# Optimization experiments

Measured on AMD Instinct MI355X. Metric: run time of the kernel, lower is better.

## Reference

```python
import jax, jax.numpy as jnp
import numpy as np

H = 768
NH = 12
HD = H // NH  # 64


def setup_inputs() -> dict:
    key = jax.random.key(0)
    ks = jax.random.split(key, 8)
    B, S = 4, 2048
    sc = 1.0 / np.sqrt(H)
    return {
        "hidden_states": jax.random.normal(ks[0], (B, S, H), dtype=jnp.float32),
        "attention_mask": jnp.zeros((B, 1, 1, S), dtype=jnp.float32),
        "Wq": jax.random.normal(ks[1], (H, H), dtype=jnp.float32) * sc,
        "bq": jnp.zeros((H,), dtype=jnp.float32),
        "Wk": jax.random.normal(ks[2], (H, H), dtype=jnp.float32) * sc,
        "bk": jnp.zeros((H,), dtype=jnp.float32),
        "Wv": jax.random.normal(ks[3], (H, H), dtype=jnp.float32) * sc,
        "bv": jnp.zeros((H,), dtype=jnp.float32),
    }


def _split_heads(x):
    # [B,S,H] -> [B,NH,S,HD]
    B, S, _ = x.shape
    return x.reshape(B, S, NH, HD).transpose(0, 2, 1, 3)


def reference(hidden_states, attention_mask, Wq, bq, Wk, bk, Wv, bv):
    q = _split_heads(hidden_states @ Wq + bq)
    k = _split_heads(hidden_states @ Wk + bk)
    v = _split_heads(hidden_states @ Wv + bv)
    # scores: [B,NH,S,S]
    scores = jnp.einsum("bhqd,bhkd->bhqk", q, k) / np.sqrt(HD)
    scores = scores + attention_mask
    probs = jax.nn.softmax(scores, axis=-1)  # dropout is identity in eval
    ctx = jnp.einsum("bhqk,bhkd->bhqd", probs, v)
    B, _, S, _ = ctx.shape
    return ctx.transpose(0, 2, 1, 3).reshape(B, S, H)
```

## Files before the change

### kernel.cpp

```cpp
#include <hip/hip_runtime.h>
#include <stdint.h>

typedef short bf16x8 __attribute__((ext_vector_type(8)));
typedef float f32x4  __attribute__((ext_vector_type(4)));
typedef unsigned short u16;

#define B_  4
#define S_  2048
#define H_  768
#define NH_ 12
#define HD_ 64
#define NPROJ_N (3*H_)
#define PSW 72

static __device__ __forceinline__ u16 f2bf(float f) {
    union { float f; unsigned int u; } x; x.f = f;
    return (u16)((x.u + 0x8000u) >> 16);
}
static __device__ __forceinline__ bf16x8 ld8(const u16* p) {
    return *(const bf16x8*)(const void*)p;
}
static __device__ __forceinline__ void st8(u16* p, bf16x8 v) {
    *(bf16x8*)(void*)p = v;
}
static __device__ __forceinline__ void async_ld16(const u16* g, const short* l) {
    __builtin_amdgcn_global_load_lds(
        (__attribute__((address_space(1))) void*)g,
        (__attribute__((address_space(3))) void*)l,
        16, 0, 0);
}

__global__ __launch_bounds__(256) void conv_hidden(const float* __restrict__ in,
                                                   u16* __restrict__ out) {
    int i = (blockIdx.x * 256 + threadIdx.x) * 4;
    float4 v = *(const float4*)(in + i);
    ushort4 o;
    o.x = f2bf(v.x); o.y = f2bf(v.y); o.z = f2bf(v.z); o.w = f2bf(v.w);
    *(ushort4*)(out + i) = o;
}

__global__ __launch_bounds__(256) void conv_w(const float* __restrict__ wq,
                                              const float* __restrict__ wk,
                                              const float* __restrict__ wv,
                                              u16* __restrict__ wt) {
    __shared__ float t[32][33];
    const int proj = blockIdx.z;
    const float* w = (proj == 0) ? wq : (proj == 1) ? wk : wv;
    u16* o = wt + (size_t)proj * H_ * H_;
    const int tx = threadIdx.x, ty = threadIdx.y;
    const int n0 = blockIdx.x * 32, k0 = blockIdx.y * 32;
    #pragma unroll
    for (int i = 0; i < 4; i++)
        t[ty + i * 8][tx] = w[(size_t)(k0 + ty + i * 8) * H_ + n0 + tx];
    __syncthreads();
    #pragma unroll
    for (int i = 0; i < 4; i++)
        o[(size_t)(n0 + ty + i * 8) * H_ + k0 + tx] = f2bf(t[tx][ty + i * 8]);
}

__global__ __launch_bounds__(256) void qkv_gemm(const u16* __restrict__ A,
                                                const u16* __restrict__ Wt,
                                                const float* __restrict__ bq,
                                                const float* __restrict__ bk,
                                                const float* __restrict__ bv,
                                                u16* __restrict__ qo,
                                                u16* __restrict__ ko,
                                                u16* __restrict__ vto) {
    __shared__ alignas(16) short SMEM[128 * 128];
    short* As = SMEM;
    short* Bs = SMEM + 128 * 64;

    const int tid  = threadIdx.x;
    const int wave = tid >> 6;
    const int lane = tid & 63;
    const int quad = lane >> 4;
    const int l16  = lane & 15;
    const int wm   = wave & 1;
    const int wn   = wave >> 1;

    const int m0 = blockIdx.x * 128;
    const int n0 = blockIdx.y * 128;

    int stR[4], stC[4];
    #pragma unroll
    for (int j = 0; j < 4; j++) {
        const int lc = wave * 256 + j * 64 + lane;
        stR[j] = lc >> 3;
        stC[j] = ((lc & 7) ^ (stR[j] & 7)) * 8;
    }
    const int fx0 = ((quad ^ (l16 & 7))) * 8;
    const int fx1 = fx0 ^ 32;

    f32x4 acc[4][4];
    #pragma unroll
    for (int i = 0; i < 4; i++)
        #pragma unroll
        for (int j = 0; j < 4; j++) acc[i][j] = (f32x4)0.0f;

    for (int kt = 0; kt < 12; kt++) {
        const int kk = kt * 64;
        __syncthreads();
        #pragma unroll
        for (int j = 0; j < 4; j++) {
            async_ld16(A  + (size_t)(m0 + stR[j]) * H_ + kk + stC[j], &As[(wave * 256 + j * 64) * 8]);
            async_ld16(Wt + (size_t)(n0 + stR[j]) * H_ + kk + stC[j], &Bs[(wave * 256 + j * 64) * 8]);
        }
        __syncthreads();
        #pragma unroll
        for (int ks = 0; ks < 2; ks++) {
            const int fx = ks ? fx1 : fx0;
            bf16x8 af[4], bfr[4];
            #pragma unroll
            for (int i = 0; i < 4; i++)
                af[i] = *(const bf16x8*)(const void*)&As[(wm * 64 + i * 16 + l16) * 64 + fx];
            #pragma unroll
            for (int j = 0; j < 4; j++)
                bfr[j] = *(const bf16x8*)(const void*)&Bs[(wn * 64 + j * 16 + l16) * 64 + fx];
            #pragma unroll
            for (int i = 0; i < 4; i++)
                #pragma unroll
                for (int j = 0; j < 4; j++)
                    acc[i][j] = __builtin_amdgcn_mfma_f32_16x16x32_bf16(af[i], bfr[j], acc[i][j], 0, 0, 0);
        }
    }

    const int proj  = n0 / H_;
    const int hbase = (n0 % H_) >> 6;
    const float* bias = (proj == 0) ? bq : (proj == 1) ? bk : bv;

    __syncthreads();

    #pragma unroll
    for (int nj = 0; nj < 4; nj++) {
        const int nl = wn * 64 + nj * 16 + l16;
        const float bv_ = bias[(n0 % H_) + nl];
        #pragma unroll
        for (int mi = 0; mi < 4; mi++) {
            #pragma unroll
            for (int r = 0; r < 4; r++) {
                const int ml = wm * 64 + mi * 16 + quad * 4 + r;
                const u16 val = f2bf(acc[mi][nj][r] + bv_);
                if (proj < 2)
                    ((u16*)SMEM)[ml * 128 + ((nl + (ml & 15) * 8) & 127)] = val;
                else
                    ((u16*)SMEM)[nl * 128 + ((ml + (nl & 15) * 8) & 127)] = val;
            }
        }
    }
    __syncthreads();

    if (proj < 2) {
        u16* dst0 = (proj == 0) ? qo : ko;
        const int c = tid & 7;
        #pragma unroll
        for (int j = 0; j < 8; j++) {
            const int idx = j * 32 + (tid >> 3);
            const int ml = idx >> 1, h2 = idx & 1;
            const int nbase = h2 * 64 + c * 8;
            bf16x8 v8 = *(const bf16x8*)(const void*)&((u16*)SMEM)[ml * 128 + ((nbase + (ml & 15) * 8) & 127)];
            const int m = m0 + ml;
            const int b = m >> 11, s = m & 2047;
            st8(dst0 + ((size_t)(b * NH_ + hbase + h2) * S_ + s) * HD_ + c * 8, v8);
        }
    } else {
        const int b = m0 >> 11;
        #pragma unroll
        for (int j = 0; j < 8; j++) {
            const int nl = (tid >> 3) + (j & 3) * 32;
            const int c  = (tid & 7) + (j >> 2) * 8;
            bf16x8 v8 = *(const bf16x8*)(const void*)&((u16*)SMEM)[nl * 128 + ((c * 8 + (nl & 15) * 8) & 127)];
            const int h2 = nl >> 6, d = nl & 63;
            st8(vto + ((size_t)(b * NH_ + hbase + h2) * HD_ + d) * S_ + (m0 & 2047) + c * 8, v8);
        }
    }
}

__global__ __launch_bounds__(256) void attn_kernel(const u16* __restrict__ q,
                                                   const u16* __restrict__ k,
                                                   const u16* __restrict__ vt,
                                                   const float* __restrict__ mask,
                                                   float* __restrict__ out) {
    __shared__ alignas(16) short Ks[2][64 * 64];
    __shared__ alignas(16) short Vs[2][64 * 64];
    __shared__ alignas(16) short Ps[64 * PSW];

    const int tid  = threadIdx.x;
    const int wave = tid >> 6;
    const int lane = tid & 63;
    const int quad = lane >> 4;
    const int l16  = lane & 15;

    const int bh = blockIdx.y;
    const int b  = bh / NH_;
    const int q0 = blockIdx.x * 64;
    const float C1 = 0.125f * 1.44269504f;

    const u16* qbase = q + ((size_t)bh * S_ + q0 + wave * 16 + l16) * HD_;
    bf16x8 qf0 = ld8(qbase + quad * 8);
    bf16x8 qf1 = ld8(qbase + 32 + quad * 8);

    const u16* kbase = k  + (size_t)bh * S_ * HD_;
    const u16* vbase = vt + (size_t)bh * HD_ * S_;

    const int lc0 = wave * 128 + lane;
    const int lc1 = lc0 + 64;
    const int kOff0 = ((lc0 >> 3) * 8 + ((lc0 & 7) ^ ((lc0 >> 3) & 7))) * 8;
    const int kOff1 = ((lc1 >> 3) * 8 + ((lc1 & 7) ^ ((lc1 >> 3) & 7))) * 8;
    const int vRow0 = lc0 >> 3, vRow1 = lc1 >> 3;
    const int vOff0 = ((lc0 & 7) ^ (vRow0 & 7)) * 8;
    const int vOff1 = ((lc1 & 7) ^ (vRow1 & 7)) * 8;
    const int fx0 = (quad ^ (l16 & 7)) * 8;
    const int fx1 = fx0 ^ 32;

    float lsum[4] = {0.f, 0.f, 0.f, 0.f};
    f32x4 o_acc[4];
    #pragma unroll
    for (int c = 0; c < 4; c++) o_acc[c] = (f32x4)0.0f;

#define STAGE(kt_, buf_)                                                                       \
    do {                                                                                       \
        async_ld16(kbase + (size_t)(kt_) * 4096 + kOff0,           &Ks[buf_][wave * 1024]);        \
        async_ld16(kbase + (size_t)(kt_) * 4096 + kOff1,           &Ks[buf_][wave * 1024 + 512]);  \
        async_ld16(vbase + (size_t)vRow0 * S_ + (kt_) * 64 + vOff0, &Vs[buf_][wave * 1024]);       \
        async_ld16(vbase + (size_t)vRow1 * S_ + (kt_) * 64 + vOff1, &Vs[buf_][wave * 1024 + 512]); \
    } while (0)

    STAGE(0, 0);
    __syncthreads();

    for (int kt = 0; kt < S_ / 64; kt++) {
        const int cur = kt & 1;
        if (kt + 1 < S_ / 64) STAGE(kt + 1, cur ^ 1);
        const int kk = kt * 64;
        const short* Kc = Ks[cur];
        const short* Vc = Vs[cur];

        f32x4 sacc[4];
        #pragma unroll
        for (int c = 0; c < 4; c++) sacc[c] = (f32x4)0.0f;
        #pragma unroll
        for (int c = 0; c < 4; c++) {
            bf16x8 kf0 = *(const bf16x8*)(const void*)&Kc[(c * 16 + l16) * 64 + fx0];
            sacc[c] = __builtin_amdgcn_mfma_f32_16x16x32_bf16(qf0, kf0, sacc[c], 0, 0, 0);
            bf16x8 kf1 = *(const bf16x8*)(const void*)&Kc[(c * 16 + l16) * 64 + fx1];
            sacc[c] = __builtin_amdgcn_mfma_f32_16x16x32_bf16(qf1, kf1, sacc[c], 0, 0, 0);
        }

        float pv[4][4];
        #pragma unroll
        for (int c = 0; c < 4; c++) {
            const float ml = mask[(size_t)b * S_ + kk + c * 16 + l16] * 1.44269504f;
            #pragma unroll
            for (int r = 0; r < 4; r++) {
                const float p = __builtin_amdgcn_exp2f(sacc[c][r] * C1 + ml);
                pv[c][r] = p;
                lsum[r] += p;
            }
        }

        u16* Pw = (u16*)Ps;
        #pragma unroll
        for (int c = 0; c < 4; c++)
            #pragma unroll
            for (int r = 0; r < 4; r++)
                Pw[(wave * 16 + quad * 4 + r) * PSW + c * 16 + l16] = f2bf(pv[c][r]);

        bf16x8 pa0 = *(const bf16x8*)(const void*)&Ps[(wave * 16 + l16) * PSW + quad * 8];
        bf16x8 pa1 = *(const bf16x8*)(const void*)&Ps[(wave * 16 + l16) * PSW + 32 + quad * 8];
        #pragma unroll
        for (int c2 = 0; c2 < 4; c2++) {
            bf16x8 vb0 = *(const bf16x8*)(const void*)&Vc[(c2 * 16 + l16) * 64 + fx0];
            o_acc[c2] = __builtin_amdgcn_mfma_f32_16x16x32_bf16(pa0, vb0, o_acc[c2], 0, 0, 0);
            bf16x8 vb1 = *(const bf16x8*)(const void*)&Vc[(c2 * 16 + l16) * 64 + fx1];
            o_acc[c2] = __builtin_amdgcn_mfma_f32_16x16x32_bf16(pa1, vb1, o_acc[c2], 0, 0, 0);
        }
        __syncthreads();
    }
#undef STAGE

    const int h = bh % NH_;
    #pragma unroll
    for (int r = 0; r < 4; r++) {
        float l = lsum[r];
        #pragma unroll
        for (int off = 1; off < 16; off <<= 1) l += __shfl_xor(l, off);
        const float linv = 1.0f / l;
        const int s = q0 + wave * 16 + quad * 4 + r;
        #pragma unroll
        for (int c2 = 0; c2 < 4; c2++) {
            const int d = c2 * 16 + l16;
            out[((size_t)b * S_ + s) * H_ + h * 64 + d] = o_acc[c2][r] * linv;
        }
    }
}

extern "C" void kernel_launch(void* const* d_in, const int* in_sizes, int n_in,
                              void* d_out, int out_size, void* d_ws, size_t ws_size,
                              hipStream_t stream) {
    const float* hidden = (const float*)d_in[0];
    const float* amask  = (const float*)d_in[1];
    const float* Wq     = (const float*)d_in[2];
    const float* bq     = (const float*)d_in[3];
    const float* Wk     = (const float*)d_in[4];
    const float* bk     = (const float*)d_in[5];
    const float* Wv     = (const float*)d_in[6];
    const float* bv     = (const float*)d_in[7];
    float* out = (float*)d_out;

    char* ws = (char*)d_ws;
    const size_t sz_hidden = (size_t)B_ * S_ * H_ * 2;
    const size_t sz_wt     = (size_t)NPROJ_N * H_ * 2;
    const size_t sz_qkv    = (size_t)B_ * S_ * H_ * 2;

    u16* hid_bf = (u16*)(ws);
    u16* wt     = (u16*)(ws + sz_hidden);
    u16* qbuf   = (u16*)(ws + sz_hidden + sz_wt);
    u16* kbuf   = (u16*)(ws + sz_hidden + sz_wt + sz_qkv);
    u16* vtbuf  = (u16*)(ws + sz_hidden + sz_wt + 2 * sz_qkv);

    conv_hidden<<<dim3((B_ * S_ * H_) / 1024), dim3(256), 0, stream>>>(hidden, hid_bf);
    conv_w<<<dim3(H_ / 32, H_ / 32, 3), dim3(32, 8), 0, stream>>>(Wq, Wk, Wv, wt);
    qkv_gemm<<<dim3((B_ * S_) / 128, NPROJ_N / 128), dim3(256), 0, stream>>>(
        hid_bf, wt, bq, bk, bv, qbuf, kbuf, vtbuf);
    attn_kernel<<<dim3(S_ / 64, B_ * NH_), dim3(256), 0, stream>>>(
        qbuf, kbuf, vtbuf, amask, out);
}
```

Before: 247.5 us.

## Double-buffer QKV GEMM tiles and enlarge attention blocks to 128 queries

```diff
diff --git a/kernel.cpp b/kernel.cpp
--- a/kernel.cpp
+++ b/kernel.cpp
@@ -66,9 +66,7 @@
                                                 u16* __restrict__ qo,
                                                 u16* __restrict__ ko,
                                                 u16* __restrict__ vto) {
-    __shared__ alignas(16) short SMEM[128 * 128];
-    short* As = SMEM;
-    short* Bs = SMEM + 128 * 64;
+    __shared__ alignas(16) short SMEM[4][128 * 64];
 
     const int tid  = threadIdx.x;
     const int wave = tid >> 6;
@@ -88,7 +86,7 @@
         stR[j] = lc >> 3;
         stC[j] = ((lc & 7) ^ (stR[j] & 7)) * 8;
     }
-    const int fx0 = ((quad ^ (l16 & 7))) * 8;
+    const int fx0 = (quad ^ (l16 & 7)) * 8;
     const int fx1 = fx0 ^ 32;
 
     f32x4 acc[4][4];
@@ -97,15 +95,26 @@
         #pragma unroll
         for (int j = 0; j < 4; j++) acc[i][j] = (f32x4)0.0f;
 
+#define GSTAGE(kt_, buf_)                                                                     \
+    do {                                                                                      \
+        const int kk_ = (kt_) * 64;                                                           \
+        _Pragma("unroll")                                                                     \
+        for (int j = 0; j < 4; j++) {                                                         \
+            async_ld16(A  + (size_t)(m0 + stR[j]) * H_ + kk_ + stC[j],                        \
+                       &SMEM[(buf_) * 2][(wave * 256 + j * 64) * 8]);                         \
+            async_ld16(Wt + (size_t)(n0 + stR[j]) * H_ + kk_ + stC[j],                        \
+                       &SMEM[(buf_) * 2 + 1][(wave * 256 + j * 64) * 8]);                     \
+        }                                                                                     \
+    } while (0)
+
+    GSTAGE(0, 0);
+    __syncthreads();
+
     for (int kt = 0; kt < 12; kt++) {
-        const int kk = kt * 64;
-        __syncthreads();
-        #pragma unroll
-        for (int j = 0; j < 4; j++) {
-            async_ld16(A  + (size_t)(m0 + stR[j]) * H_ + kk + stC[j], &As[(wave * 256 + j * 64) * 8]);
-            async_ld16(Wt + (size_t)(n0 + stR[j]) * H_ + kk + stC[j], &Bs[(wave * 256 + j * 64) * 8]);
-        }
-        __syncthreads();
+        const int cur = kt & 1;
+        if (kt + 1 < 12) GSTAGE(kt + 1, cur ^ 1);
+        const short* As = SMEM[cur * 2];
+        const short* Bs = SMEM[cur * 2 + 1];
         #pragma unroll
         for (int ks = 0; ks < 2; ks++) {
             const int fx = ks ? fx1 : fx0;
@@ -122,13 +131,14 @@
                 for (int j = 0; j < 4; j++)
                     acc[i][j] = __builtin_amdgcn_mfma_f32_16x16x32_bf16(af[i], bfr[j], acc[i][j], 0, 0, 0);
         }
-    }
+        __syncthreads();
+    }
+#undef GSTAGE
 
     const int proj  = n0 / H_;
     const int hbase = (n0 % H_) >> 6;
     const float* bias = (proj == 0) ? bq : (proj == 1) ? bk : bv;
-
-    __syncthreads();
+    u16* Ct = (u16*)SMEM;
 
     #pragma unroll
     for (int nj = 0; nj < 4; nj++) {
@@ -141,9 +151,9 @@
                 const int ml = wm * 64 + mi * 16 + quad * 4 + r;
                 const u16 val = f2bf(acc[mi][nj][r] + bv_);
                 if (proj < 2)
-                    ((u16*)SMEM)[ml * 128 + ((nl + (ml & 15) * 8) & 127)] = val;
+                    Ct[ml * 128 + ((nl + (ml & 15) * 8) & 127)] = val;
                 else
-                    ((u16*)SMEM)[nl * 128 + ((ml + (nl & 15) * 8) & 127)] = val;
+                    Ct[nl * 128 + ((ml + (nl & 15) * 8) & 127)] = val;
             }
         }
     }
@@ -157,7 +167,7 @@
             const int idx = j * 32 + (tid >> 3);
             const int ml = idx >> 1, h2 = idx & 1;
             const int nbase = h2 * 64 + c * 8;
-            bf16x8 v8 = *(const bf16x8*)(const void*)&((u16*)SMEM)[ml * 128 + ((nbase + (ml & 15) * 8) & 127)];
+            bf16x8 v8 = *(const bf16x8*)(const void*)&Ct[ml * 128 + ((nbase + (ml & 15) * 8) & 127)];
             const int m = m0 + ml;
             const int b = m >> 11, s = m & 2047;
             st8(dst0 + ((size_t)(b * NH_ + hbase + h2) * S_ + s) * HD_ + c * 8, v8);
@@ -168,21 +178,21 @@
         for (int j = 0; j < 8; j++) {
             const int nl = (tid >> 3) + (j & 3) * 32;
             const int c  = (tid & 7) + (j >> 2) * 8;
-            bf16x8 v8 = *(const bf16x8*)(const void*)&((u16*)SMEM)[nl * 128 + ((c * 8 + (nl & 15) * 8) & 127)];
+            bf16x8 v8 = *(const bf16x8*)(const void*)&Ct[nl * 128 + ((c * 8 + (nl & 15) * 8) & 127)];
             const int h2 = nl >> 6, d = nl & 63;
             st8(vto + ((size_t)(b * NH_ + hbase + h2) * HD_ + d) * S_ + (m0 & 2047) + c * 8, v8);
         }
     }
 }
 
-__global__ __launch_bounds__(256) void attn_kernel(const u16* __restrict__ q,
+__global__ __launch_bounds__(512) void attn_kernel(const u16* __restrict__ q,
                                                    const u16* __restrict__ k,
                                                    const u16* __restrict__ vt,
                                                    const float* __restrict__ mask,
                                                    float* __restrict__ out) {
     __shared__ alignas(16) short Ks[2][64 * 64];
     __shared__ alignas(16) short Vs[2][64 * 64];
-    __shared__ alignas(16) short Ps[64 * PSW];
+    __shared__ alignas(16) short Ps[128 * PSW];
 
     const int tid  = threadIdx.x;
     const int wave = tid >> 6;
@@ -190,9 +200,9 @@
     const int quad = lane >> 4;
     const int l16  = lane & 15;
 
-    const int bh = blockIdx.y;
+    const int bh = blockIdx.x;
     const int b  = bh / NH_;
-    const int q0 = blockIdx.x * 64;
+    const int q0 = blockIdx.y * 128;
     const float C1 = 0.125f * 1.44269504f;
 
     const u16* qbase = q + ((size_t)bh * S_ + q0 + wave * 16 + l16) * HD_;
@@ -202,13 +212,9 @@
     const u16* kbase = k  + (size_t)bh * S_ * HD_;
     const u16* vbase = vt + (size_t)bh * HD_ * S_;
 
-    const int lc0 = wave * 128 + lane;
-    const int lc1 = lc0 + 64;
-    const int kOff0 = ((lc0 >> 3) * 8 + ((lc0 & 7) ^ ((lc0 >> 3) & 7))) * 8;
-    const int kOff1 = ((lc1 >> 3) * 8 + ((lc1 & 7) ^ ((lc1 >> 3) & 7))) * 8;
-    const int vRow0 = lc0 >> 3, vRow1 = lc1 >> 3;
-    const int vOff0 = ((lc0 & 7) ^ (vRow0 & 7)) * 8;
-    const int vOff1 = ((lc1 & 7) ^ (vRow1 & 7)) * 8;
+    const int sRow = tid >> 3;
+    const int sCol = ((tid & 7) ^ (sRow & 7)) * 8;
+    const int kOff = sRow * 64 + sCol;
     const int fx0 = (quad ^ (l16 & 7)) * 8;
     const int fx1 = fx0 ^ 32;
 
@@ -217,12 +223,10 @@
     #pragma unroll
     for (int c = 0; c < 4; c++) o_acc[c] = (f32x4)0.0f;
 
-#define STAGE(kt_, buf_)                                                                       \
-    do {                                                                                       \
-        async_ld16(kbase + (size_t)(kt_) * 4096 + kOff0,           &Ks[buf_][wave * 1024]);        \
-        async_ld16(kbase + (size_t)(kt_) * 4096 + kOff1,           &Ks[buf_][wave * 1024 + 512]);  \
-        async_ld16(vbase + (size_t)vRow0 * S_ + (kt_) * 64 + vOff0, &Vs[buf_][wave * 1024]);       \
-        async_ld16(vbase + (size_t)vRow1 * S_ + (kt_) * 64 + vOff1, &Vs[buf_][wave * 1024 + 512]); \
+#define STAGE(kt_, buf_)                                                              \
+    do {                                                                              \
+        async_ld16(kbase + (size_t)(kt_) * 4096 + kOff,        &Ks[buf_][wave * 512]); \
+        async_ld16(vbase + (size_t)sRow * S_ + (kt_) * 64 + sCol, &Vs[buf_][wave * 512]); \
     } while (0)
 
     STAGE(0, 0);
@@ -322,6 +326,6 @@
     conv_w<<<dim3(H_ / 32, H_ / 32, 3), dim3(32, 8), 0, stream>>>(Wq, Wk, Wv, wt);
     qkv_gemm<<<dim3((B_ * S_) / 128, NPROJ_N / 128), dim3(256), 0, stream>>>(
         hid_bf, wt, bq, bk, bv, qbuf, kbuf, vtbuf);
-    attn_kernel<<<dim3(S_ / 64, B_ * NH_), dim3(256), 0, stream>>>(
+    attn_kernel<<<dim3(B_ * NH_, S_ / 128), dim3(512), 0, stream>>>(
         qbuf, kbuf, vtbuf, amask, out);
 }
```

After: 217.0 us. -12.3%, faster.
